# Kernel optimization log

Hardware: AMD Instinct MI355X
Metric: run time of the kernel (lower is better)

The kernel has to match this reference:

```python
import jax, jax.numpy as jnp
import numpy as np

HEADS = 16
DIM_HEAD = 64
SCALE = DIM_HEAD ** -0.5


def setup_inputs() -> dict:
    key = jax.random.key(0)
    ks = jax.random.split(key, 7)
    b, n, m, d = 2, 2048, 2048, 1024
    inner = HEADS * DIM_HEAD  # 1024
    patch_embed = jax.random.normal(ks[0], (b, n, d), dtype=jnp.float32)
    pixel_embed = jax.random.normal(ks[1], (b, m, d), dtype=jnp.float32)
    s = 1.0 / np.sqrt(d)
    Wq = jax.random.normal(ks[2], (d, inner), dtype=jnp.float32) * s
    Wk = jax.random.normal(ks[3], (d, inner), dtype=jnp.float32) * s
    Wv = jax.random.normal(ks[4], (d, inner), dtype=jnp.float32) * s
    Wo = jax.random.normal(ks[5], (inner, d), dtype=jnp.float32) * (1.0 / np.sqrt(inner))
    bo = jax.random.normal(ks[6], (d,), dtype=jnp.float32) * 0.01
    return {"patch_embed": patch_embed, "pixel_embed": pixel_embed,
            "Wq": Wq, "Wk": Wk, "Wv": Wv, "Wo": Wo, "bo": bo}


def reference(patch_embed, pixel_embed, Wq, Wk, Wv, Wo, bo):
    b, n, _ = patch_embed.shape
    h, dh = HEADS, DIM_HEAD
    # projections
    q = patch_embed @ Wq  # [b, n, h*dh]
    k = pixel_embed @ Wk  # [b, m, h*dh]
    v = pixel_embed @ Wv  # [b, m, h*dh]
    # split heads: [b, seq, h, dh]
    q = q.reshape(b, n, h, dh)
    k = k.reshape(b, -1, h, dh)
    v = v.reshape(b, -1, h, dh)
    sim = jnp.einsum('bihd,bjhd->bhij', q, k) * SCALE  # [b, h, n, m]
    attn = jax.nn.softmax(sim, axis=-1)
    out = jnp.einsum('bhij,bjhd->bihd', attn, v)  # [b, n, h, dh]
    out = out.reshape(b, n, h * dh)
    return out @ Wo + bo  # [b, n, query_dim]
```

## Files before the change

### kernel.cpp

```cpp
#include <hip/hip_runtime.h>

#define SEQ 2048
#define DMODEL 1024
#define HEADS 16
#define DH 64
#define QSCALE 0.180336880f

typedef __attribute__((ext_vector_type(8))) short short8;
typedef __attribute__((ext_vector_type(4))) float f32x4;

__device__ __forceinline__ ushort f2bf(float x) {
  union { float f; unsigned u; } v; v.f = x;
  return (ushort)((v.u + 0x7fffu + ((v.u >> 16) & 1u)) >> 16);
}

__device__ __forceinline__ void gld16(const ushort* g, ushort* l) {
  __builtin_amdgcn_global_load_lds(
      (const __attribute__((address_space(1))) unsigned int*)g,
      (__attribute__((address_space(3))) unsigned int*)l, 16, 0, 0);
}

__device__ __forceinline__ size_t qk_idx(int bh, int s, int d) {
  return ((((size_t)bh * (SEQ / 16) + (s >> 4)) * 2 + (d >> 5)) * 64 +
          ((d >> 3) & 3) * 16 + (s & 15)) * 8 + (d & 7);
}
__device__ __forceinline__ size_t v_idx(int bh, int s, int d) {
  return ((((size_t)bh * 4 + (d >> 4)) * (SEQ / 32) + (s >> 5)) * 64 +
          ((s >> 3) & 3) * 16 + (d & 15)) * 8 + (s & 7);
}

__global__ __launch_bounds__(256) void prologue(
    const float* __restrict__ patch, const float* __restrict__ pixel,
    const float* __restrict__ W0, const float* __restrict__ W1,
    const float* __restrict__ W2, const float* __restrict__ W3,
    ushort* __restrict__ pb, ushort* __restrict__ xb,
    ushort* __restrict__ O0, ushort* __restrict__ O1,
    ushort* __restrict__ O2, ushort* __restrict__ O3) {
  const int z = blockIdx.z;
  const int tx = threadIdx.x, ty = threadIdx.y;
  if (z < 2) {
    const float4* in = (const float4*)(z ? pixel : patch);
    ushort4* out = (ushort4*)(z ? xb : pb);
    const int base = (blockIdx.y * 32 + blockIdx.x) * 256 + ty * 32 + tx;
#pragma unroll
    for (int rep = 0; rep < 4; ++rep) {
      const int i = base + rep * 262144;
      float4 f = in[i];
      out[i] = make_ushort4(f2bf(f.x), f2bf(f.y), f2bf(f.z), f2bf(f.w));
    }
    return;
  }
  __shared__ float tile[32][33];
  const int zz = z - 2;
  const float* in = zz == 0 ? W0 : zz == 1 ? W1 : zz == 2 ? W2 : W3;
  ushort* out = zz == 0 ? O0 : zz == 1 ? O1 : zz == 2 ? O2 : O3;
  const float scale = zz == 0 ? QSCALE : 1.0f;
  const int n0 = blockIdx.x * 32, k0 = blockIdx.y * 32;
#pragma unroll
  for (int i = 0; i < 4; ++i)
    tile[ty + i * 8][tx] = in[(size_t)(k0 + ty + i * 8) * DMODEL + n0 + tx];
  __syncthreads();
#pragma unroll
  for (int i = 0; i < 4; ++i)
    out[(size_t)(n0 + ty + i * 8) * DMODEL + k0 + tx] =
        f2bf(tile[tx][ty + i * 8] * scale);
}

__global__ __launch_bounds__(256) void mfma_gemm_qkv(
    const ushort* __restrict__ pb, const ushort* __restrict__ xb,
    const ushort* __restrict__ wqt, const ushort* __restrict__ wkt,
    const ushort* __restrict__ wvt, ushort* __restrict__ qws,
    ushort* __restrict__ kws, ushort* __restrict__ vws) {
  __shared__ __align__(16) ushort As[128 * 64];
  __shared__ __align__(16) ushort Bs[128 * 64];
  const int z = blockIdx.z;
  const ushort* A = (z == 0) ? pb : xb;
  const ushort* Bt = (z == 0) ? wqt : (z == 1) ? wkt : wvt;

  const int t = threadIdx.x;
  const int w = t >> 6, lane = t & 63, ln = lane & 15, q = lane >> 4;
  const int wm = w & 1, wn = w >> 1;
  const int row0 = blockIdx.y * 128, col0 = blockIdx.x * 128;
  const int sw = ln & 7;

  f32x4 acc[4][4];
#pragma unroll
  for (int i = 0; i < 4; ++i)
#pragma unroll
    for (int j = 0; j < 4; ++j) acc[i][j] = (f32x4){0.f, 0.f, 0.f, 0.f};

  for (int k0 = 0; k0 < DMODEL; k0 += 64) {
    __syncthreads();
#pragma unroll
    for (int rep = 0; rep < 4; ++rep) {
      const int u0 = rep * 256 + w * 64;
      const int u = u0 + lane;
      const int r = u >> 3, gl = (u & 7) ^ (r & 7);
      gld16(&A[(size_t)(row0 + r) * DMODEL + k0 + gl * 8], &As[u0 * 8]);
      gld16(&Bt[(size_t)(col0 + r) * DMODEL + k0 + gl * 8], &Bs[u0 * 8]);
    }
    __syncthreads();
#pragma unroll
    for (int ks = 0; ks < 2; ++ks) {
      short8 af[4], bf[4];
#pragma unroll
      for (int rt = 0; rt < 4; ++rt)
        af[rt] = *(const short8*)&As[(wm * 64 + rt * 16 + ln) * 64 +
                                     (((ks * 4 + q) ^ sw) * 8)];
#pragma unroll
      for (int ct = 0; ct < 4; ++ct)
        bf[ct] = *(const short8*)&Bs[(wn * 64 + ct * 16 + ln) * 64 +
                                     (((ks * 4 + q) ^ sw) * 8)];
#pragma unroll
      for (int rt = 0; rt < 4; ++rt)
#pragma unroll
        for (int ct = 0; ct < 4; ++ct)
          acc[rt][ct] = __builtin_amdgcn_mfma_f32_16x16x32_bf16(af[rt], bf[ct],
                                                                acc[rt][ct], 0, 0, 0);
    }
  }

  if (z < 2) {
    ushort* dst = z == 0 ? qws : kws;
#pragma unroll
    for (int rt = 0; rt < 4; ++rt)
#pragma unroll
      for (int ct = 0; ct < 4; ++ct) {
        const int c = col0 + wn * 64 + ct * 16 + ln;
        const int h = c >> 6, d = c & 63;
#pragma unroll
        for (int reg = 0; reg < 4; ++reg) {
          const int r = row0 + wm * 64 + rt * 16 + q * 4 + reg;
          const int b = r >> 11, s = r & (SEQ - 1);
          dst[qk_idx(b * HEADS + h, s, d)] = f2bf(acc[rt][ct][reg]);
        }
      }
  } else {
#pragma unroll
    for (int rt = 0; rt < 4; ++rt)
#pragma unroll
      for (int ct = 0; ct < 4; ++ct) {
        const int c = col0 + wn * 64 + ct * 16 + ln;
        const int h = c >> 6, d = c & 63;
        const int r0 = row0 + wm * 64 + rt * 16 + q * 4;
        const int b = r0 >> 11, s0 = r0 & (SEQ - 1);
        ushort4 u4 = make_ushort4(f2bf(acc[rt][ct][0]), f2bf(acc[rt][ct][1]),
                                  f2bf(acc[rt][ct][2]), f2bf(acc[rt][ct][3]));
        *(ushort4*)&vws[v_idx(b * HEADS + h, s0, d)] = u4;
      }
  }
}

__global__ __launch_bounds__(256) void flash_mfma(
    const ushort* __restrict__ Qg, const ushort* __restrict__ Kg,
    const ushort* __restrict__ Vg, float* __restrict__ PO0,
    float* __restrict__ PO1, float* __restrict__ L0, float* __restrict__ L1) {
  __shared__ __align__(16) ushort Ps[64 * 72];

  const int t = threadIdx.x;
  const int w = t >> 6, lane = t & 63, ln = lane & 15, q = lane >> 4;
  const int qt = blockIdx.x;
  const int bh = blockIdx.y;
  const int seg = blockIdx.z;

  float* __restrict__ PO = seg ? PO1 : PO0;
  float* __restrict__ Lb = seg ? L1 : L0;

  const ushort* qg = Qg + (size_t)bh * SEQ * DH;
  const ushort* kg = Kg + (size_t)bh * SEQ * DH;
  const ushort* vg = Vg + (size_t)bh * DH * SEQ;

  short8 qf[2];
#pragma unroll
  for (int ks = 0; ks < 2; ++ks)
    qf[ks] = *(const short8*)&qg[((((size_t)(qt * 4 + w)) * 2 + ks) * 64 + lane) * 8];

  float l_i[4] = {0.f, 0.f, 0.f, 0.f};
  f32x4 acc_o[4];
#pragma unroll
  for (int nt = 0; nt < 4; ++nt) acc_o[nt] = (f32x4){0.f, 0.f, 0.f, 0.f};

  for (int kt = seg * 16; kt < seg * 16 + 16; ++kt) {
    short8 bv[2][4];
#pragma unroll
    for (int ks2 = 0; ks2 < 2; ++ks2)
#pragma unroll
      for (int nt = 0; nt < 4; ++nt)
        bv[ks2][nt] = *(const short8*)&vg[(((size_t)nt * (SEQ / 32) + kt * 2 + ks2) *
                                           64 + lane) * 8];

    f32x4 accs[4];
#pragma unroll
    for (int ct = 0; ct < 4; ++ct) accs[ct] = (f32x4){0.f, 0.f, 0.f, 0.f};
#pragma unroll
    for (int ks = 0; ks < 2; ++ks) {
      short8 bfr[4];
#pragma unroll
      for (int ct = 0; ct < 4; ++ct)
        bfr[ct] = *(const short8*)&kg[((((size_t)(kt * 4 + ct)) * 2 + ks) * 64 +
                                       lane) * 8];
#pragma unroll
      for (int ct = 0; ct < 4; ++ct)
        accs[ct] = __builtin_amdgcn_mfma_f32_16x16x32_bf16(qf[ks], bfr[ct],
                                                           accs[ct], 0, 0, 0);
    }

#pragma unroll
    for (int ct = 0; ct < 4; ++ct)
#pragma unroll
      for (int reg = 0; reg < 4; ++reg) {
        const float p = __builtin_amdgcn_exp2f(accs[ct][reg]);
        l_i[reg] += p;
        Ps[(w * 16 + q * 4 + reg) * 72 + ct * 16 + ln] = f2bf(p);
      }

#pragma unroll
    for (int ks2 = 0; ks2 < 2; ++ks2) {
      const short8 pa = *(const short8*)&Ps[(w * 16 + ln) * 72 + ks2 * 32 + q * 8];
#pragma unroll
      for (int nt = 0; nt < 4; ++nt)
        acc_o[nt] = __builtin_amdgcn_mfma_f32_16x16x32_bf16(pa, bv[ks2][nt],
                                                            acc_o[nt], 0, 0, 0);
    }
  }

#pragma unroll
  for (int reg = 0; reg < 4; ++reg) {
    float l = l_i[reg];
    l += __shfl_xor(l, 1, 16);
    l += __shfl_xor(l, 2, 16);
    l += __shfl_xor(l, 4, 16);
    l += __shfl_xor(l, 8, 16);
    const int s = qt * 64 + w * 16 + q * 4 + reg;
    if (ln == 0) Lb[bh * SEQ + s] = l;
#pragma unroll
    for (int nt = 0; nt < 4; ++nt)
      PO[((size_t)bh * SEQ + s) * DH + nt * 16 + ln] = acc_o[nt][reg];
  }
}

__global__ __launch_bounds__(256) void merge_reduce(
    const float4* __restrict__ PO0, const float4* __restrict__ PO1,
    const float* __restrict__ L0, const float* __restrict__ L1,
    ushort* __restrict__ aws) {
  const int i = blockIdx.x * 256 + threadIdx.x;
  const int row = i >> 4, d4 = i & 15;
  const int bh = row >> 11, s = row & (SEQ - 1);
  const int b = bh >> 4, h = bh & 15;
  const float4 a = PO0[i];
  const float4 c = PO1[i];
  const float inv = 1.0f / (L0[row] + L1[row]);
  ushort4 u = make_ushort4(f2bf((a.x + c.x) * inv), f2bf((a.y + c.y) * inv),
                           f2bf((a.z + c.z) * inv), f2bf((a.w + c.w) * inv));
  *(ushort4*)&aws[((size_t)b * SEQ + s) * DMODEL + h * DH + d4 * 4] = u;
}

__global__ __launch_bounds__(256) void mfma_gemm_out(const ushort* __restrict__ A,
                                                     const ushort* __restrict__ Bt,
                                                     const float* __restrict__ bias,
                                                     float* __restrict__ dst) {
  __shared__ __align__(16) ushort As[64 * 64];
  __shared__ __align__(16) ushort Bs[128 * 64];
  const int t = threadIdx.x;
  const int w = t >> 6, lane = t & 63, ln = lane & 15, q = lane >> 4;
  const int wm = w & 1, wn = w >> 1;
  const int row0 = blockIdx.y * 64, col0 = blockIdx.x * 128;
  const int sw = ln & 7;

  f32x4 acc[2][4];
#pragma unroll
  for (int i = 0; i < 2; ++i)
#pragma unroll
    for (int j = 0; j < 4; ++j) acc[i][j] = (f32x4){0.f, 0.f, 0.f, 0.f};

  for (int k0 = 0; k0 < DMODEL; k0 += 64) {
    __syncthreads();
#pragma unroll
    for (int rep = 0; rep < 2; ++rep) {
      const int u0 = rep * 256 + w * 64;
      const int u = u0 + lane;
      const int r = u >> 3, gl = (u & 7) ^ (r & 7);
      gld16(&A[(size_t)(row0 + r) * DMODEL + k0 + gl * 8], &As[u0 * 8]);
    }
#pragma unroll
    for (int rep = 0; rep < 4; ++rep) {
      const int u0 = rep * 256 + w * 64;
      const int u = u0 + lane;
      const int r = u >> 3, gl = (u & 7) ^ (r & 7);
      gld16(&Bt[(size_t)(col0 + r) * DMODEL + k0 + gl * 8], &Bs[u0 * 8]);
    }
    __syncthreads();
#pragma unroll
    for (int ks = 0; ks < 2; ++ks) {
      short8 af[2], bf[4];
#pragma unroll
      for (int rt = 0; rt < 2; ++rt)
        af[rt] = *(const short8*)&As[(wm * 32 + rt * 16 + ln) * 64 +
                                     (((ks * 4 + q) ^ sw) * 8)];
#pragma unroll
      for (int ct = 0; ct < 4; ++ct)
        bf[ct] = *(const short8*)&Bs[(wn * 64 + ct * 16 + ln) * 64 +
                                     (((ks * 4 + q) ^ sw) * 8)];
#pragma unroll
      for (int rt = 0; rt < 2; ++rt)
#pragma unroll
        for (int ct = 0; ct < 4; ++ct)
          acc[rt][ct] = __builtin_amdgcn_mfma_f32_16x16x32_bf16(af[rt], bf[ct],
                                                                acc[rt][ct], 0, 0, 0);
    }
  }

#pragma unroll
  for (int rt = 0; rt < 2; ++rt)
#pragma unroll
    for (int ct = 0; ct < 4; ++ct) {
      const int c = col0 + wn * 64 + ct * 16 + ln;
      const float bi = bias[c];
#pragma unroll
      for (int reg = 0; reg < 4; ++reg) {
        const int r = row0 + wm * 32 + rt * 16 + q * 4 + reg;
        dst[(size_t)r * DMODEL + c] = acc[rt][ct][reg] + bi;
      }
    }
}

extern "C" void kernel_launch(void* const* d_in, const int* in_sizes, int n_in,
                              void* d_out, int out_size, void* d_ws,
                              size_t ws_size, hipStream_t stream) {
  const float* patch = (const float*)d_in[0];
  const float* pixel = (const float*)d_in[1];
  const float* Wq = (const float*)d_in[2];
  const float* Wk = (const float*)d_in[3];
  const float* Wv = (const float*)d_in[4];
  const float* Wo = (const float*)d_in[5];
  const float* bo = (const float*)d_in[6];
  float* out = (float*)d_out;

  const size_t E = (size_t)2 * SEQ * DMODEL;
  const size_t W = (size_t)DMODEL * DMODEL;
  ushort* pb  = (ushort*)d_ws;
  ushort* xb  = pb + E;
  ushort* wqt = xb + E;
  ushort* wkt = wqt + W;
  ushort* wvt = wkt + W;
  ushort* wot = wvt + W;
  ushort* qws = wot + W;
  ushort* kws = qws + E;
  ushort* vws = kws + E;
  ushort* aws = vws + E;

  float* PO0 = (float*)pb;
  float* PO1 = out;
  float* L0 = (float*)wqt;
  float* L1 = L0 + 32 * SEQ;

  prologue<<<dim3(32, 32, 6), dim3(32, 8), 0, stream>>>(
      patch, pixel, Wq, Wk, Wv, Wo, pb, xb, wqt, wkt, wvt, wot);
  mfma_gemm_qkv<<<dim3(8, 32, 3), 256, 0, stream>>>(pb, xb, wqt, wkt, wvt,
                                                    qws, kws, vws);
  flash_mfma<<<dim3(32, 32, 2), 256, 0, stream>>>(qws, kws, vws, PO0, PO1, L0, L1);
  merge_reduce<<<dim3((32 * SEQ * DH / 4) / 256), 256, 0, stream>>>(
      (const float4*)PO0, (const float4*)PO1, L0, L1, aws);
  mfma_gemm_out<<<dim3(8, 64), 256, 0, stream>>>(aws, wot, bo, out);
}
```

Measured before the change: 226.1 us.

## Stage K/V tiles in LDS and process two query tiles per wave

The flash attention kernel now has each wave handle two 16-row query tiles, so each block covers 128 query rows and the grid is halved. K and V fragments for each key tile are loaded once per block into LDS with async global-to-LDS loads and shared across waves, instead of every wave reading them from global memory. The per-block LDS footprint and register use grow, and the bf16 rounding of P changes to round-half-up; two barriers per iteration add synchronisation with no double buffering.

```diff
diff --git a/kernel.cpp b/kernel.cpp
--- a/kernel.cpp
+++ b/kernel.cpp
@@ -151,11 +151,13 @@
   }
 }
 
-__global__ __launch_bounds__(256) void flash_mfma(
+__global__ __launch_bounds__(256, 4) void flash_mfma(
     const ushort* __restrict__ Qg, const ushort* __restrict__ Kg,
     const ushort* __restrict__ Vg, float* __restrict__ PO0,
     float* __restrict__ PO1, float* __restrict__ L0, float* __restrict__ L1) {
-  __shared__ __align__(16) ushort Ps[64 * 72];
+  __shared__ __align__(16) ushort Kst[8 * 512];
+  __shared__ __align__(16) ushort Vst[8 * 512];
+  __shared__ __align__(16) ushort Ps[128 * 72];
 
   const int t = threadIdx.x;
   const int w = t >> 6, lane = t & 63, ln = lane & 15, q = lane >> 4;
@@ -170,73 +172,102 @@
   const ushort* kg = Kg + (size_t)bh * SEQ * DH;
   const ushort* vg = Vg + (size_t)bh * DH * SEQ;
 
-  short8 qf[2];
-#pragma unroll
-  for (int ks = 0; ks < 2; ++ks)
-    qf[ks] = *(const short8*)&qg[((((size_t)(qt * 4 + w)) * 2 + ks) * 64 + lane) * 8];
-
-  float l_i[4] = {0.f, 0.f, 0.f, 0.f};
-  f32x4 acc_o[4];
-#pragma unroll
-  for (int nt = 0; nt < 4; ++nt) acc_o[nt] = (f32x4){0.f, 0.f, 0.f, 0.f};
+  short8 qf[2][2];
+#pragma unroll
+  for (int rt = 0; rt < 2; ++rt)
+#pragma unroll
+    for (int ks = 0; ks < 2; ++ks)
+      qf[rt][ks] = *(const short8*)
+          &qg[(((size_t)(qt * 8 + w * 2 + rt) * 2 + ks) * 64 + lane) * 8];
+
+  float l_i[2][4];
+  f32x4 acc_o[2][4];
+#pragma unroll
+  for (int rt = 0; rt < 2; ++rt)
+#pragma unroll
+    for (int reg = 0; reg < 4; ++reg) l_i[rt][reg] = 0.f;
+#pragma unroll
+  for (int rt = 0; rt < 2; ++rt)
+#pragma unroll
+    for (int nt = 0; nt < 4; ++nt) acc_o[rt][nt] = (f32x4){0.f, 0.f, 0.f, 0.f};
 
   for (int kt = seg * 16; kt < seg * 16 + 16; ++kt) {
-    short8 bv[2][4];
-#pragma unroll
-    for (int ks2 = 0; ks2 < 2; ++ks2)
+    __syncthreads();
+#pragma unroll
+    for (int i = 0; i < 4; ++i) {
+      const int f = w * 4 + i;
+      if (f < 8) {
+        gld16(&kg[((size_t)(kt * 8 + f)) * 512 + lane * 8], &Kst[f * 512]);
+      } else {
+        const int f2 = f - 8, nt = f2 >> 1, ks2 = f2 & 1;
+        gld16(&vg[((size_t)(nt * (SEQ / 32) + kt * 2 + ks2)) * 512 + lane * 8],
+              &Vst[f2 * 512]);
+      }
+    }
+    __syncthreads();
+
+    f32x4 accs[2][4];
+#pragma unroll
+    for (int rt = 0; rt < 2; ++rt)
+#pragma unroll
+      for (int ct = 0; ct < 4; ++ct) accs[rt][ct] = (f32x4){0.f, 0.f, 0.f, 0.f};
+#pragma unroll
+    for (int ks = 0; ks < 2; ++ks)
+#pragma unroll
+      for (int ct = 0; ct < 4; ++ct) {
+        const short8 bf = *(const short8*)&Kst[(ct * 2 + ks) * 512 + lane * 8];
+#pragma unroll
+        for (int rt = 0; rt < 2; ++rt)
+          accs[rt][ct] = __builtin_amdgcn_mfma_f32_16x16x32_bf16(
+              qf[rt][ks], bf, accs[rt][ct], 0, 0, 0);
+      }
+
+#pragma unroll
+    for (int rt = 0; rt < 2; ++rt)
+#pragma unroll
+      for (int ct = 0; ct < 4; ++ct)
+#pragma unroll
+        for (int reg = 0; reg < 4; ++reg) {
+          const float p = __builtin_amdgcn_exp2f(accs[rt][ct][reg]);
+          l_i[rt][reg] += p;
+          union { float f; unsigned u; } v; v.f = p;
+          Ps[(w * 32 + rt * 16 + q * 4 + reg) * 72 + ct * 16 + ln] =
+              (ushort)((v.u + 0x8000u) >> 16);
+        }
+
+#pragma unroll
+    for (int ks2 = 0; ks2 < 2; ++ks2) {
+      short8 pa[2];
+#pragma unroll
+      for (int rt = 0; rt < 2; ++rt)
+        pa[rt] = *(const short8*)&Ps[(w * 32 + rt * 16 + ln) * 72 +
+                                     ks2 * 32 + q * 8];
+#pragma unroll
+      for (int nt = 0; nt < 4; ++nt) {
+        const short8 bv = *(const short8*)&Vst[(nt * 2 + ks2) * 512 + lane * 8];
+#pragma unroll
+        for (int rt = 0; rt < 2; ++rt)
+          acc_o[rt][nt] = __builtin_amdgcn_mfma_f32_16x16x32_bf16(
+              pa[rt], bv, acc_o[rt][nt], 0, 0, 0);
+      }
+    }
+  }
+
+#pragma unroll
+  for (int rt = 0; rt < 2; ++rt)
+#pragma unroll
+    for (int reg = 0; reg < 4; ++reg) {
+      float l = l_i[rt][reg];
+      l += __shfl_xor(l, 1, 16);
+      l += __shfl_xor(l, 2, 16);
+      l += __shfl_xor(l, 4, 16);
+      l += __shfl_xor(l, 8, 16);
+      const int s = qt * 128 + w * 32 + rt * 16 + q * 4 + reg;
+      if (ln == 0) Lb[bh * SEQ + s] = l;
 #pragma unroll
       for (int nt = 0; nt < 4; ++nt)
-        bv[ks2][nt] = *(const short8*)&vg[(((size_t)nt * (SEQ / 32) + kt * 2 + ks2) *
-                                           64 + lane) * 8];
-
-    f32x4 accs[4];
-#pragma unroll
-    for (int ct = 0; ct < 4; ++ct) accs[ct] = (f32x4){0.f, 0.f, 0.f, 0.f};
-#pragma unroll
-    for (int ks = 0; ks < 2; ++ks) {
-      short8 bfr[4];
-#pragma unroll
-      for (int ct = 0; ct < 4; ++ct)
-        bfr[ct] = *(const short8*)&kg[((((size_t)(kt * 4 + ct)) * 2 + ks) * 64 +
-                                       lane) * 8];
-#pragma unroll
-      for (int ct = 0; ct < 4; ++ct)
-        accs[ct] = __builtin_amdgcn_mfma_f32_16x16x32_bf16(qf[ks], bfr[ct],
-                                                           accs[ct], 0, 0, 0);
-    }
-
-#pragma unroll
-    for (int ct = 0; ct < 4; ++ct)
-#pragma unroll
-      for (int reg = 0; reg < 4; ++reg) {
-        const float p = __builtin_amdgcn_exp2f(accs[ct][reg]);
-        l_i[reg] += p;
-        Ps[(w * 16 + q * 4 + reg) * 72 + ct * 16 + ln] = f2bf(p);
-      }
-
-#pragma unroll
-    for (int ks2 = 0; ks2 < 2; ++ks2) {
-      const short8 pa = *(const short8*)&Ps[(w * 16 + ln) * 72 + ks2 * 32 + q * 8];
-#pragma unroll
-      for (int nt = 0; nt < 4; ++nt)
-        acc_o[nt] = __builtin_amdgcn_mfma_f32_16x16x32_bf16(pa, bv[ks2][nt],
-                                                            acc_o[nt], 0, 0, 0);
-    }
-  }
-
-#pragma unroll
-  for (int reg = 0; reg < 4; ++reg) {
-    float l = l_i[reg];
-    l += __shfl_xor(l, 1, 16);
-    l += __shfl_xor(l, 2, 16);
-    l += __shfl_xor(l, 4, 16);
-    l += __shfl_xor(l, 8, 16);
-    const int s = qt * 64 + w * 16 + q * 4 + reg;
-    if (ln == 0) Lb[bh * SEQ + s] = l;
-#pragma unroll
-    for (int nt = 0; nt < 4; ++nt)
-      PO[((size_t)bh * SEQ + s) * DH + nt * 16 + ln] = acc_o[nt][reg];
-  }
+        PO[((size_t)bh * SEQ + s) * DH + nt * 16 + ln] = acc_o[rt][nt][reg];
+    }
 }
 
 __global__ __launch_bounds__(256) void merge_reduce(
@@ -358,7 +389,7 @@
       patch, pixel, Wq, Wk, Wv, Wo, pb, xb, wqt, wkt, wvt, wot);
   mfma_gemm_qkv<<<dim3(8, 32, 3), 256, 0, stream>>>(pb, xb, wqt, wkt, wvt,
                                                     qws, kws, vws);
-  flash_mfma<<<dim3(32, 32, 2), 256, 0, stream>>>(qws, kws, vws, PO0, PO1, L0, L1);
+  flash_mfma<<<dim3(16, 32, 2), 256, 0, stream>>>(qws, kws, vws, PO0, PO1, L0, L1);
   merge_reduce<<<dim3((32 * SEQ * DH / 4) / 256), 256, 0, stream>>>(
       (const float4*)PO0, (const float4*)PO1, L0, L1, aws);
   mfma_gemm_out<<<dim3(8, 64), 256, 0, stream>>>(aws, wot, bo, out);
```

New measurement: 207.8 us. 8.1% less time.
